# Kernel tuning notes

Hardware: AMD Instinct MI355X
Metric: run time of the kernel (lower is better)

Reference implementation:

```python
import jax, jax.numpy as jnp
import numpy as np

N_NODES = 100000
BN_EPS = 1e-5


def _gcn_layer(x, W, b, row, col, ew):
    # support = x @ W  (dense GEMM), then sparse aggregation: out[r] += w * support[c]
    support = x @ W
    msgs = ew[:, None] * support[col]            # [E, out_dim] gather
    agg = jax.ops.segment_sum(msgs, row, num_segments=N_NODES)
    return agg + b


def _batch_norm(x):
    # fresh BatchNorm1d each call: training-mode batch stats, gamma=1, beta=0
    mean = jnp.mean(x, axis=0, keepdims=True)
    var = jnp.var(x, axis=0, keepdims=True)      # biased variance, as in BN
    return (x - mean) * jax.lax.rsqrt(var + BN_EPS)


def setup_inputs() -> dict:
    key = jax.random.key(0)
    ks = jax.random.split(key, 10)
    nfeat, nhid, nclass = 512, 256, 64
    E = 3200000
    x = jax.random.normal(ks[0], (N_NODES, nfeat), dtype=jnp.float32)
    edge_index = jax.random.randint(ks[1], (2, E), 0, N_NODES, dtype=jnp.int32)
    edge_weight = jax.random.uniform(ks[2], (E,), dtype=jnp.float32)
    def glorot(k, fan_in, fan_out):
        s = 1.0 / np.sqrt(fan_in)
        return jax.random.uniform(k, (fan_in, fan_out), dtype=jnp.float32, minval=-s, maxval=s)
    W1 = glorot(ks[3], nfeat, nhid)
    b1 = jnp.zeros((nhid,), dtype=jnp.float32)
    W2 = glorot(ks[4], nhid, nhid)
    b2 = jnp.zeros((nhid,), dtype=jnp.float32)
    W3 = glorot(ks[5], nhid, nclass)
    b3 = jnp.zeros((nclass,), dtype=jnp.float32)
    return {"x": x, "edge_index": edge_index, "edge_weight": edge_weight,
            "W1": W1, "b1": b1, "W2": W2, "b2": b2, "W3": W3, "b3": b3}


def reference(x, edge_index, edge_weight, W1, b1, W2, b2, W3, b3):
    row, col = edge_index[0], edge_index[1]
    h = _batch_norm(jax.nn.relu(_gcn_layer(x, W1, b1, row, col, edge_weight)))
    h = _batch_norm(jax.nn.relu(_gcn_layer(h, W2, b2, row, col, edge_weight)))
    h = jax.nn.relu(_gcn_layer(h, W3, b3, row, col, edge_weight))
    return h
```

## Files before the change

kernel.cpp:

```cpp
#include <hip/hip_runtime.h>

#define THREADS 256
#define BSH 7
#define EPB 8192

typedef _Float16 f16;
typedef _Float16 f16x8 __attribute__((ext_vector_type(8)));
typedef _Float16 f16x4 __attribute__((ext_vector_type(4)));
typedef float f32x4 __attribute__((ext_vector_type(4)));


__global__ __launch_bounds__(256) void k_hist_convW(
    const int* __restrict__ rows, int* __restrict__ cnt2d, int e, int nblk, int nb,
    const float* __restrict__ W, f16* __restrict__ Wt, int K, int N,
    float* __restrict__ statZero, unsigned long long* __restrict__ tpub, int ntiles) {
  int t = threadIdx.x;
  if (blockIdx.x < nblk) {
    __shared__ int hist[1024];
    int blk = blockIdx.x;
    for (int i = t; i < nb; i += 256) hist[i] = 0;
    __syncthreads();
    int eb = blk * EPB;
#pragma unroll 4
    for (int it = 0; it < 32; ++it) {
      int i = eb + it * 256 + t;
      if (i < e) atomicAdd(&hist[rows[i] >> BSH], 1);
    }
    __syncthreads();
    for (int i = t; i < nb; i += 256) cnt2d[i * nblk + blk] = hist[i];
  } else {
    int cb = blockIdx.x - nblk;
    if (cb == 0) {
#pragma unroll
      for (int j = 0; j < 6; ++j) statZero[j * 256 + t] = 0.f;
      for (int i = t; i < ntiles; i += 256) tpub[i] = 0ULL;
    }
    int i = cb * 256 + t;
    if (i < N * K) {
      int n = i / K, k = i - n * K;
      Wt[i] = (f16)W[(size_t)k * N + n];
    }
  }
}


__global__ __launch_bounds__(256) void k_scanDL(
    const int* __restrict__ cnt, int* __restrict__ outp,
    unsigned long long* __restrict__ tpub, int n) {
  __shared__ int sh[256];
  __shared__ int sPrefix;
  int tile = blockIdx.x, t = threadIdx.x;
  int base = tile * 1024 + t * 4;
  int v[4];
#pragma unroll
  for (int j = 0; j < 4; ++j) {
    int idx = base + j;
    v[j] = (idx < n) ? cnt[idx] : 0;
  }
  int tot = v[0] + v[1] + v[2] + v[3];
  sh[t] = tot;
  __syncthreads();
  for (int off = 1; off < 256; off <<= 1) {
    int x = 0;
    if (t >= off) x = sh[t - off];
    __syncthreads();
    sh[t] += x;
    __syncthreads();
  }
  int blockTot = sh[255];
  int run = sh[t] - tot;

  if (t == 0) {
    if (tile == 0) {
      sPrefix = 0;
      atomicExch(&tpub[0], ((unsigned long long)(unsigned)blockTot << 2) | 2ULL);
    } else {
      atomicExch(&tpub[tile], ((unsigned long long)(unsigned)blockTot << 2) | 1ULL);
      long long sum = 0;
      int pred = tile - 1;
      while (true) {
        unsigned long long s = atomicAdd(&tpub[pred], 0ULL);
        unsigned st = (unsigned)(s & 3ULL);
        if (st == 2) { sum += (long long)(s >> 2); break; }
        if (st == 1) { sum += (long long)(s >> 2); --pred; }
      }
      sPrefix = (int)sum;
      atomicExch(&tpub[tile],
                 ((unsigned long long)(unsigned)(sum + blockTot) << 2) | 2ULL);
    }
  }
  __syncthreads();
  int pfx = sPrefix;
#pragma unroll
  for (int j = 0; j < 4; ++j) {
    int idx = base + j;
    if (idx < n) outp[idx] = run + pfx;
    run += v[j];
  }
  if (tile == gridDim.x - 1 && t == 0) outp[n] = pfx + blockTot;
}


template <int BN, bool AF16>
__device__ __forceinline__ void gemm_dev(
    int mblk, const void* __restrict__ Ap, const f16* __restrict__ Wt,
    const float* __restrict__ biasRow, f16* __restrict__ Csup, int M, int K,
    char* smem) {
  constexpr int BM = 128;
  constexpr int BK = 32;
  constexpr int LDT = BK + 8;
  f16 (*As)[LDT] = (f16(*)[LDT])smem;
  f16 (*Bs)[LDT] = (f16(*)[LDT])(smem + BM * LDT * 2);

  const int tid = threadIdx.x;
  const int wave = tid >> 6;
  const int lane = tid & 63;
  const int m0 = mblk * BM;
  constexpr int WM = (BN == 256) ? 8 : 2;
  constexpr int WN = 4;
  const int wrow = (BN == 256) ? 0 : wave * 32;
  const int wcol = (BN == 256) ? wave * 64 : 0;
  const int l15 = lane & 15;
  const int lq = lane >> 4;

  const int arow = tid >> 1;
  const int akofs = (tid & 1) * 16;
  const int srow = tid >> 2;
  const int skofs = (tid & 3) * 8;
  constexpr int BROWS = BN / 64;

  f32x4 acc[WM][WN] = {};

  for (int k0 = 0; k0 < K; k0 += BK) {
    f16x8 a16[2];
    int gr = m0 + arow;
    if constexpr (AF16) {
      if (gr < M) {
        const f16* ap = (const f16*)Ap + (size_t)gr * K + k0 + akofs;
        a16[0] = *(const f16x8*)ap;
        a16[1] = *(const f16x8*)(ap + 8);
      } else {
#pragma unroll
        for (int j = 0; j < 8; ++j) { a16[0][j] = (f16)0.f; a16[1][j] = (f16)0.f; }
      }
    } else {
      float va[16];
      if (gr < M) {
        const float* ap = (const float*)Ap + (size_t)gr * K + k0 + akofs;
#pragma unroll
        for (int q = 0; q < 4; ++q) *(float4*)&va[q * 4] = *(const float4*)(ap + q * 4);
      } else {
#pragma unroll
        for (int j = 0; j < 16; ++j) va[j] = 0.f;
      }
#pragma unroll
      for (int j = 0; j < 8; ++j) { a16[0][j] = (f16)va[j]; a16[1][j] = (f16)va[8 + j]; }
    }

    f16x8 vb[BROWS];
#pragma unroll
    for (int j = 0; j < BROWS; ++j)
      vb[j] = *(const f16x8*)(Wt + (size_t)(srow + j * 64) * K + k0 + skofs);

    __syncthreads();
    *(f16x8*)&As[arow][akofs] = a16[0];
    *(f16x8*)&As[arow][akofs + 8] = a16[1];
#pragma unroll
    for (int j = 0; j < BROWS; ++j) *(f16x8*)&Bs[srow + j * 64][skofs] = vb[j];
    __syncthreads();

    f16x8 af[WM], bf[WN];
#pragma unroll
    for (int m = 0; m < WM; ++m)
      af[m] = *(const f16x8*)&As[wrow + m * 16 + l15][lq * 8];
#pragma unroll
    for (int n = 0; n < WN; ++n)
      bf[n] = *(const f16x8*)&Bs[wcol + n * 16 + l15][lq * 8];
#pragma unroll
    for (int m = 0; m < WM; ++m)
#pragma unroll
      for (int n = 0; n < WN; ++n)
        acc[m][n] = __builtin_amdgcn_mfma_f32_16x16x32_f16(af[m], bf[n], acc[m][n], 0, 0, 0);
  }

  float bb[WN];
#pragma unroll
  for (int n = 0; n < WN; ++n)
    bb[n] = biasRow ? biasRow[wcol + n * 16 + l15] : 0.f;

#pragma unroll
  for (int m = 0; m < WM; ++m) {
#pragma unroll
    for (int r = 0; r < 4; ++r) {
      int row = m0 + wrow + m * 16 + lq * 4 + r;
      if (row < M) {
        f16* cp = Csup + (size_t)row * BN + wcol + l15;
#pragma unroll
        for (int n = 0; n < WN; ++n) cp[n * 16] = (f16)(acc[m][n][r] + bb[n]);
      }
    }
  }
}

template <int BN, bool AF16>
__global__ __launch_bounds__(256) void k_gemm_mfma(
    const void* __restrict__ Ap, const f16* __restrict__ Wt,
    const float* __restrict__ biasRow, f16* __restrict__ Csup, int M, int K) {
  __shared__ __align__(16) char smem[(128 + BN) * 40 * 2];
  gemm_dev<BN, AF16>(blockIdx.x, Ap, Wt, biasRow, Csup, M, K, smem);
}


__global__ __launch_bounds__(256) void k_bin_gemm(
    const int* __restrict__ rows, const int* __restrict__ cols,
    const float* __restrict__ w, const int* __restrict__ off2d,
    int2* __restrict__ temp, int e, int nblk, int nb,
    const float* __restrict__ x, const f16* __restrict__ Wt1,
    f16* __restrict__ sup, int M) {
  __shared__ __align__(16) char smem[(128 + 256) * 40 * 2];
  int t = threadIdx.x;
  if (blockIdx.x < nblk) {
    int* base = (int*)smem;
    int* cursor = (int*)smem + 1024;
    int blk = blockIdx.x;
    for (int i = t; i < nb; i += 256) {
      base[i] = off2d[i * nblk + blk];
      cursor[i] = 0;
    }
    __syncthreads();
    int eb = blk * EPB;
#pragma unroll 4
    for (int it = 0; it < 32; ++it) {
      int i = eb + it * 256 + t;
      if (i < e) {
        int r = rows[i];
        int b = r >> BSH;
        int pos = base[b] + atomicAdd(&cursor[b], 1);
        temp[pos] = make_int2(((r & 127) << 17) | cols[i], __float_as_int(w[i]));
      }
    }
  } else {
    gemm_dev<256, false>(blockIdx.x - nblk, x, Wt1, nullptr, sup, M, 512, smem);
  }
}


__global__ __launch_bounds__(256) void k_scatter(
    const int2* __restrict__ temp, const int* __restrict__ off2d,
    int* __restrict__ rowptr, int2* __restrict__ ed,
    int n, int e, int nblk, int nb) {
  __shared__ int rowCnt[128];
  __shared__ int rowBase[128];
  __shared__ int rowCur[128];
  int b = blockIdx.x, t = threadIdx.x;
  int r0 = b << BSH;
  int nr = min(128, n - r0);
  int start = off2d[b * nblk];
  int end = off2d[(b + 1) * nblk];
  if (t < 128) rowCnt[t] = 0;
  __syncthreads();
  for (int p = start + t; p < end; p += 256)
    atomicAdd(&rowCnt[temp[p].x >> 17], 1);
  __syncthreads();
  int v = 0;
  if (t < 128) {
    v = rowCnt[t];
    rowBase[t] = v;
  }
  __syncthreads();
  for (int off = 1; off < 128; off <<= 1) {
    int x = 0;
    if (t < 128 && t >= off) x = rowBase[t - off];
    __syncthreads();
    if (t < 128) rowBase[t] += x;
    __syncthreads();
  }
  if (t < 128) {
    int excl = rowBase[t] - v;
    rowBase[t] = excl;
    rowCur[t] = 0;
    if (t < nr) rowptr[r0 + t] = start + excl;
  }
  if (b == nb - 1 && t == 0) rowptr[n] = e;
  __syncthreads();
  for (int p = start + t; p < end; p += 256) {
    int2 ei = temp[p];
    int ro = ei.x >> 17;
    int slot = start + rowBase[ro] + atomicAdd(&rowCur[ro], 1);
    ed[slot] = make_int2(ei.x & 0x1FFFF, ei.y);
  }
}


__global__ __launch_bounds__(256) void k_bnfold(
    const float* __restrict__ W, const float* __restrict__ sums,
    f16* __restrict__ Wt, float* __restrict__ biasRow, int K, int N, int n) {
  __shared__ float sc[256], sf[256];
  int t = threadIdx.x;
  if (t < K) {
    float inv = 1.0f / (float)n;
    float mean = sums[t] * inv;
    float var = sums[256 + t] * inv - mean * mean;
    float rstd = rsqrtf(var + 1e-5f);
    sc[t] = rstd;
    sf[t] = -mean * rstd;
  }
  __syncthreads();
  int i = blockIdx.x * 256 + t;
  if (i < N * K) {
    int nn = i / K, k = i - nn * K;
    Wt[i] = (f16)(sc[k] * W[(size_t)k * N + nn]);
  }
  if (blockIdx.x < (K >> 4) && t < N) {
    int k0 = blockIdx.x * 16;
    float s = 0.f;
#pragma unroll
    for (int j = 0; j < 16; ++j) s += sf[k0 + j] * W[(size_t)(k0 + j) * N + t];
    atomicAdd(&biasRow[t], s);
  }
}


__global__ __launch_bounds__(256) void k_agg256(
    const f16* __restrict__ sup, const int* __restrict__ rowptr,
    const int2* __restrict__ ed, const float* __restrict__ bias,
    f16* __restrict__ out, int n) {
  int wid = (blockIdx.x * THREADS + threadIdx.x) >> 6;
  int lane = threadIdx.x & 63;
  if (wid >= n) return;
  int p0 = rowptr[wid], p1 = rowptr[wid + 1];

  const f16x4* supv = (const f16x4*)sup;
  float acc[4][4] = {};
  int p = p0;
  for (; p + 16 <= p1; p += 16) {
    int2 e[16];
#pragma unroll
    for (int j = 0; j < 16; ++j) e[j] = ed[p + j];
    f16x4 v[16];
#pragma unroll
    for (int j = 0; j < 16; ++j) v[j] = supv[(size_t)e[j].x * 64 + lane];
#pragma unroll
    for (int j = 0; j < 16; ++j) {
      float wt = __int_as_float(e[j].y);
      acc[j & 3][0] += wt * (float)v[j][0];
      acc[j & 3][1] += wt * (float)v[j][1];
      acc[j & 3][2] += wt * (float)v[j][2];
      acc[j & 3][3] += wt * (float)v[j][3];
    }
  }
  for (; p + 4 <= p1; p += 4) {
    int2 e[4];
#pragma unroll
    for (int j = 0; j < 4; ++j) e[j] = ed[p + j];
    f16x4 v[4];
#pragma unroll
    for (int j = 0; j < 4; ++j) v[j] = supv[(size_t)e[j].x * 64 + lane];
#pragma unroll
    for (int j = 0; j < 4; ++j) {
      float wt = __int_as_float(e[j].y);
      acc[j][0] += wt * (float)v[j][0];
      acc[j][1] += wt * (float)v[j][1];
      acc[j][2] += wt * (float)v[j][2];
      acc[j][3] += wt * (float)v[j][3];
    }
  }
  for (; p < p1; ++p) {
    int2 e0 = ed[p];
    float wt = __int_as_float(e0.y);
    f16x4 v = supv[(size_t)e0.x * 64 + lane];
    acc[0][0] += wt * (float)v[0];
    acc[0][1] += wt * (float)v[1];
    acc[0][2] += wt * (float)v[2];
    acc[0][3] += wt * (float)v[3];
  }
  float4 b = *(const float4*)(bias + lane * 4);
  f16x4 r;
  r[0] = (f16)fmaxf(acc[0][0] + acc[1][0] + acc[2][0] + acc[3][0] + b.x, 0.f);
  r[1] = (f16)fmaxf(acc[0][1] + acc[1][1] + acc[2][1] + acc[3][1] + b.y, 0.f);
  r[2] = (f16)fmaxf(acc[0][2] + acc[1][2] + acc[2][2] + acc[3][2] + b.z, 0.f);
  r[3] = (f16)fmaxf(acc[0][3] + acc[1][3] + acc[2][3] + acc[3][3] + b.w, 0.f);
  *(f16x4*)(out + (size_t)wid * 256 + lane * 4) = r;
}


__global__ __launch_bounds__(256) void k_agg64(
    const f16* __restrict__ sup, const int* __restrict__ rowptr,
    const int2* __restrict__ ed, const float* __restrict__ bias,
    float* __restrict__ out, int n) {
  int wid = (blockIdx.x * THREADS + threadIdx.x) >> 6;
  int lane = threadIdx.x & 63;
  if (wid >= n) return;
  int p0 = rowptr[wid], p1 = rowptr[wid + 1];
  int q = lane >> 4;
  int hl = lane & 15;

  const f16x4* supv = (const f16x4*)sup;
  float acc[2][4] = {};
  int p = p0;
  for (; p + 32 <= p1; p += 32) {
    int2 e[8];
#pragma unroll
    for (int j = 0; j < 8; ++j) e[j] = ed[p + 4 * j + q];
    f16x4 v[8];
#pragma unroll
    for (int j = 0; j < 8; ++j) v[j] = supv[(size_t)e[j].x * 16 + hl];
#pragma unroll
    for (int j = 0; j < 8; ++j) {
      float wt = __int_as_float(e[j].y);
      acc[j & 1][0] += wt * (float)v[j][0];
      acc[j & 1][1] += wt * (float)v[j][1];
      acc[j & 1][2] += wt * (float)v[j][2];
      acc[j & 1][3] += wt * (float)v[j][3];
    }
  }
  for (; p + 4 <= p1; p += 4) {
    int2 e0 = ed[p + q];
    float wt = __int_as_float(e0.y);
    f16x4 v = supv[(size_t)e0.x * 16 + hl];
    acc[0][0] += wt * (float)v[0];
    acc[0][1] += wt * (float)v[1];
    acc[0][2] += wt * (float)v[2];
    acc[0][3] += wt * (float)v[3];
  }
  if (p < p1) {
    int idx = p + q;
    int c = 0;
    float wt = 0.f;
    if (idx < p1) {
      int2 e0 = ed[idx];
      c = e0.x;
      wt = __int_as_float(e0.y);
    }
    f16x4 v = supv[(size_t)c * 16 + hl];
    acc[0][0] += wt * (float)v[0];
    acc[0][1] += wt * (float)v[1];
    acc[0][2] += wt * (float)v[2];
    acc[0][3] += wt * (float)v[3];
  }
  float t0 = acc[0][0] + acc[1][0];
  float t1 = acc[0][1] + acc[1][1];
  float t2 = acc[0][2] + acc[1][2];
  float t3 = acc[0][3] + acc[1][3];
  t0 += __shfl_xor(t0, 16); t0 += __shfl_xor(t0, 32);
  t1 += __shfl_xor(t1, 16); t1 += __shfl_xor(t1, 32);
  t2 += __shfl_xor(t2, 16); t2 += __shfl_xor(t2, 32);
  t3 += __shfl_xor(t3, 16); t3 += __shfl_xor(t3, 32);
  if (q == 0) {
    float4 b = *(const float4*)(bias + hl * 4);
    float4 res;
    res.x = fmaxf(t0 + b.x, 0.f);
    res.y = fmaxf(t1 + b.y, 0.f);
    res.z = fmaxf(t2 + b.z, 0.f);
    res.w = fmaxf(t3 + b.w, 0.f);
    *(float4*)(out + (size_t)wid * 64 + hl * 4) = res;
  }
}


__global__ __launch_bounds__(256) void k_colstats(const f16* __restrict__ y,
                                                  float* __restrict__ sums, int n) {
  __shared__ float sh[8][256];
  int t = threadIdx.x;
  int cg = (t & 31) * 8;
  int rs = t >> 5;
  float s[8] = {}, s2[8] = {};
  for (int r = blockIdx.x * 8 + rs; r < n; r += gridDim.x * 8) {
    f16x8 v = *(const f16x8*)(y + (size_t)r * 256 + cg);
#pragma unroll
    for (int j = 0; j < 8; ++j) {
      float f = (float)v[j];
      s[j] += f;
      s2[j] += f * f;
    }
  }
#pragma unroll
  for (int j = 0; j < 8; ++j) sh[rs][cg + j] = s[j];
  __syncthreads();
  float tot = 0.f;
#pragma unroll
  for (int k = 0; k < 8; ++k) tot += sh[k][t];
  atomicAdd(&sums[t], tot);
  __syncthreads();
#pragma unroll
  for (int j = 0; j < 8; ++j) sh[rs][cg + j] = s2[j];
  __syncthreads();
  tot = 0.f;
#pragma unroll
  for (int k = 0; k < 8; ++k) tot += sh[k][t];
  atomicAdd(&sums[256 + t], tot);
}


extern "C" void kernel_launch(void* const* d_in, const int* in_sizes, int n_in,
                              void* d_out, int out_size, void* d_ws, size_t ws_size,
                              hipStream_t stream) {
  const float* x = (const float*)d_in[0];
  const int* ei = (const int*)d_in[1];
  const float* ew = (const float*)d_in[2];
  const float* W1 = (const float*)d_in[3];
  const float* b1 = (const float*)d_in[4];
  const float* W2 = (const float*)d_in[5];
  const float* b2 = (const float*)d_in[6];
  const float* W3 = (const float*)d_in[7];
  const float* b3 = (const float*)d_in[8];
  float* out = (float*)d_out;

  const int N = in_sizes[0] / 512;
  const int E = in_sizes[2];

  const int NB = (N + 127) >> BSH;
  const int NBLK = (E + EPB - 1) / EPB;
  const int scanN = NB * NBLK;
  const int ntiles = (scanN + 1023) / 1024;

  char* p = (char*)d_ws;
  auto alloc = [&](size_t bytes) {
    void* r = (void*)p;
    p += (bytes + 255) & ~(size_t)255;
    return r;
  };
  int* rowptr = (int*)alloc((size_t)(N + 1) * 4);
  int* cnt2d = (int*)alloc((size_t)scanN * 4);
  int* off2d = (int*)alloc((size_t)(scanN + 1) * 4);
  unsigned long long* tpub = (unsigned long long*)alloc((size_t)ntiles * 8);
  float* statZ = (float*)alloc(1536 * 4);
  float* sumsA = statZ;
  float* sumsB = statZ + 512;
  float* biasRowA = statZ + 1024;
  float* biasRowB = statZ + 1280;
  f16* Wt1 = (f16*)alloc((size_t)512 * 256 * 2);
  f16* Wt2 = (f16*)alloc((size_t)256 * 256 * 2);
  f16* Wt3 = (f16*)alloc((size_t)256 * 64 * 2);
  int2* temp = (int2*)alloc((size_t)E * 8);
  int2* ed = (int2*)alloc((size_t)E * 8);
  f16* sup = (f16*)alloc((size_t)N * 256 * 2);
  f16* act = (f16*)alloc((size_t)N * 256 * 2);

  const int* rows = ei;
  const int* colsIn = ei + E;

  const int gemmBlocks = (N + 127) / 128;
  const int aggBlocks = (N * 64 + THREADS - 1) / THREADS;
  const int convBlocks = (512 * 256 + 255) / 256;

  k_hist_convW<<<NBLK + convBlocks, 256, 0, stream>>>(
      rows, cnt2d, E, NBLK, NB, W1, Wt1, 512, 256, statZ, tpub, ntiles);

  k_scanDL<<<ntiles, 256, 0, stream>>>(cnt2d, off2d, tpub, scanN);

  k_bin_gemm<<<NBLK + gemmBlocks, 256, 0, stream>>>(
      rows, colsIn, ew, off2d, temp, E, NBLK, NB, x, Wt1, sup, N);

  k_scatter<<<NB, 256, 0, stream>>>(temp, off2d, rowptr, ed, N, E, NBLK, NB);

  k_agg256<<<aggBlocks, 256, 0, stream>>>(sup, rowptr, ed, b1, act, N);

  k_colstats<<<240, 256, 0, stream>>>(act, sumsA, N);
  k_bnfold<<<(256 * 256 + 255) / 256, 256, 0, stream>>>(W2, sumsA, Wt2, biasRowA, 256, 256, N);

  k_gemm_mfma<256, true><<<gemmBlocks, 256, 0, stream>>>(act, Wt2, biasRowA, sup, N, 256);
  k_agg256<<<aggBlocks, 256, 0, stream>>>(sup, rowptr, ed, b2, act, N);

  k_colstats<<<240, 256, 0, stream>>>(act, sumsB, N);
  k_bnfold<<<(256 * 64 + 255) / 256, 256, 0, stream>>>(W3, sumsB, Wt3, biasRowB, 256, 64, N);

  k_gemm_mfma<64, true><<<gemmBlocks, 256, 0, stream>>>(act, Wt3, biasRowB, sup, N, 256);
  k_agg64<<<aggBlocks, 256, 0, stream>>>(sup, rowptr, ed, b3, out, N);
}
```

Before: 873.4 us.

## Fuse BN column stats into aggregation and apply BN normalization in GEMM A-load

The aggregation kernel now reduces per-column sum and sum-of-squares within each block and adds them atomically, which removes the separate colstats pass over the activation. The bnfold kernel is also removed. The GEMM instead computes per-column scale and shift from those sums and applies them to the A tile as it loads, and all three weight conversions move into the front kernel. This cuts four launches and one full read of the activations, at the cost of about 2x512 atomics per aggregation block and extra per-element ALU work plus shared-memory reads in the GEMM load path.

```diff
diff --git a/kernel.cpp b/kernel.cpp
--- a/kernel.cpp
+++ b/kernel.cpp
@@ -10,9 +10,11 @@
 typedef float f32x4 __attribute__((ext_vector_type(4)));
 
 
-__global__ __launch_bounds__(256) void k_hist_convW(
+__global__ __launch_bounds__(256) void k_front(
     const int* __restrict__ rows, int* __restrict__ cnt2d, int e, int nblk, int nb,
-    const float* __restrict__ W, f16* __restrict__ Wt, int K, int N,
+    const float* __restrict__ W1, f16* __restrict__ Wt1,
+    const float* __restrict__ W2, f16* __restrict__ Wt2,
+    const float* __restrict__ W3, f16* __restrict__ Wt3,
     float* __restrict__ statZero, unsigned long long* __restrict__ tpub, int ntiles) {
   int t = threadIdx.x;
   if (blockIdx.x < nblk) {
@@ -32,13 +34,21 @@
     int cb = blockIdx.x - nblk;
     if (cb == 0) {
 #pragma unroll
-      for (int j = 0; j < 6; ++j) statZero[j * 256 + t] = 0.f;
+      for (int j = 0; j < 4; ++j) statZero[j * 256 + t] = 0.f;
       for (int i = t; i < ntiles; i += 256) tpub[i] = 0ULL;
     }
-    int i = cb * 256 + t;
-    if (i < N * K) {
-      int n = i / K, k = i - n * K;
-      Wt[i] = (f16)W[(size_t)k * N + n];
+    if (cb < 512) {
+      int i = cb * 256 + t;
+      int n = i >> 9, k = i & 511;
+      Wt1[i] = (f16)W1[(size_t)k * 256 + n];
+    } else if (cb < 768) {
+      int i = (cb - 512) * 256 + t;
+      int n = i >> 8, k = i & 255;
+      Wt2[i] = (f16)W2[(size_t)k * 256 + n];
+    } else {
+      int i = (cb - 768) * 256 + t;
+      int n = i >> 8, k = i & 255;
+      Wt3[i] = (f16)W3[(size_t)k * 64 + n];
     }
   }
 }
@@ -101,16 +111,17 @@
 }
 
 
-template <int BN, bool AF16>
+template <int BN, bool AF16, bool BNF>
 __device__ __forceinline__ void gemm_dev(
     int mblk, const void* __restrict__ Ap, const f16* __restrict__ Wt,
-    const float* __restrict__ biasRow, f16* __restrict__ Csup, int M, int K,
-    char* smem) {
+    f16* __restrict__ Csup, int M, int K,
+    const float* __restrict__ sums, int nrows, char* smem) {
   constexpr int BM = 128;
   constexpr int BK = 32;
   constexpr int LDT = BK + 8;
   f16 (*As)[LDT] = (f16(*)[LDT])smem;
   f16 (*Bs)[LDT] = (f16(*)[LDT])(smem + BM * LDT * 2);
+  __shared__ float scL[256], sfL[256];
 
   const int tid = threadIdx.x;
   const int wave = tid >> 6;
@@ -129,6 +140,16 @@
   const int skofs = (tid & 3) * 8;
   constexpr int BROWS = BN / 64;
 
+  if constexpr (BNF) {
+    float inv = 1.0f / (float)nrows;
+    float mean = sums[tid] * inv;
+    float var = sums[256 + tid] * inv - mean * mean;
+    float rstd = rsqrtf(var + 1e-5f);
+    scL[tid] = rstd;
+    sfL[tid] = -mean * rstd;
+    __syncthreads();
+  }
+
   f32x4 acc[WM][WN] = {};
 
   for (int k0 = 0; k0 < K; k0 += BK) {
@@ -139,6 +160,15 @@
         const f16* ap = (const f16*)Ap + (size_t)gr * K + k0 + akofs;
         a16[0] = *(const f16x8*)ap;
         a16[1] = *(const f16x8*)(ap + 8);
+        if constexpr (BNF) {
+#pragma unroll
+          for (int h = 0; h < 2; ++h)
+#pragma unroll
+            for (int j = 0; j < 8; ++j) {
+              int k = k0 + akofs + h * 8 + j;
+              a16[h][j] = (f16)((float)a16[h][j] * scL[k] + sfL[k]);
+            }
+        }
       } else {
 #pragma unroll
         for (int j = 0; j < 8; ++j) { a16[0][j] = (f16)0.f; a16[1][j] = (f16)0.f; }
@@ -183,11 +213,6 @@
         acc[m][n] = __builtin_amdgcn_mfma_f32_16x16x32_f16(af[m], bf[n], acc[m][n], 0, 0, 0);
   }
 
-  float bb[WN];
-#pragma unroll
-  for (int n = 0; n < WN; ++n)
-    bb[n] = biasRow ? biasRow[wcol + n * 16 + l15] : 0.f;
-
 #pragma unroll
   for (int m = 0; m < WM; ++m) {
 #pragma unroll
@@ -196,18 +221,19 @@
       if (row < M) {
         f16* cp = Csup + (size_t)row * BN + wcol + l15;
 #pragma unroll
-        for (int n = 0; n < WN; ++n) cp[n * 16] = (f16)(acc[m][n][r] + bb[n]);
+        for (int n = 0; n < WN; ++n) cp[n * 16] = (f16)acc[m][n][r];
       }
     }
   }
 }
 
-template <int BN, bool AF16>
+template <int BN, bool AF16, bool BNF>
 __global__ __launch_bounds__(256) void k_gemm_mfma(
     const void* __restrict__ Ap, const f16* __restrict__ Wt,
-    const float* __restrict__ biasRow, f16* __restrict__ Csup, int M, int K) {
+    f16* __restrict__ Csup, int M, int K,
+    const float* __restrict__ sums, int nrows) {
   __shared__ __align__(16) char smem[(128 + BN) * 40 * 2];
-  gemm_dev<BN, AF16>(blockIdx.x, Ap, Wt, biasRow, Csup, M, K, smem);
+  gemm_dev<BN, AF16, BNF>(blockIdx.x, Ap, Wt, Csup, M, K, sums, nrows, smem);
 }
 
 
@@ -240,7 +266,7 @@
       }
     }
   } else {
-    gemm_dev<256, false>(blockIdx.x - nblk, x, Wt1, nullptr, sup, M, 512, smem);
+    gemm_dev<256, false, false>(blockIdx.x - nblk, x, Wt1, sup, M, 512, nullptr, 0, smem);
   }
 }
 
@@ -292,43 +318,18 @@
 }
 
 
-__global__ __launch_bounds__(256) void k_bnfold(
-    const float* __restrict__ W, const float* __restrict__ sums,
-    f16* __restrict__ Wt, float* __restrict__ biasRow, int K, int N, int n) {
-  __shared__ float sc[256], sf[256];
-  int t = threadIdx.x;
-  if (t < K) {
-    float inv = 1.0f / (float)n;
-    float mean = sums[t] * inv;
-    float var = sums[256 + t] * inv - mean * mean;
-    float rstd = rsqrtf(var + 1e-5f);
-    sc[t] = rstd;
-    sf[t] = -mean * rstd;
-  }
-  __syncthreads();
-  int i = blockIdx.x * 256 + t;
-  if (i < N * K) {
-    int nn = i / K, k = i - nn * K;
-    Wt[i] = (f16)(sc[k] * W[(size_t)k * N + nn]);
-  }
-  if (blockIdx.x < (K >> 4) && t < N) {
-    int k0 = blockIdx.x * 16;
-    float s = 0.f;
-#pragma unroll
-    for (int j = 0; j < 16; ++j) s += sf[k0 + j] * W[(size_t)(k0 + j) * N + t];
-    atomicAdd(&biasRow[t], s);
-  }
-}
-
-
 __global__ __launch_bounds__(256) void k_agg256(
     const f16* __restrict__ sup, const int* __restrict__ rowptr,
     const int2* __restrict__ ed, const float* __restrict__ bias,
-    f16* __restrict__ out, int n) {
-  int wid = (blockIdx.x * THREADS + threadIdx.x) >> 6;
-  int lane = threadIdx.x & 63;
-  if (wid >= n) return;
-  int p0 = rowptr[wid], p1 = rowptr[wid + 1];
+    f16* __restrict__ out, float* __restrict__ sums, int n) {
+  __shared__ float shs[4][256];
+  int tid = threadIdx.x;
+  int wave = tid >> 6;
+  int wid = (blockIdx.x * THREADS + tid) >> 6;
+  int lane = tid & 63;
+  bool valid = wid < n;
+  int p0 = 0, p1 = 0;
+  if (valid) { p0 = rowptr[wid]; p1 = rowptr[wid + 1]; }
 
   const f16x4* supv = (const f16x4*)sup;
   float acc[4][4] = {};
@@ -375,12 +376,26 @@
     acc[0][3] += wt * (float)v[3];
   }
   float4 b = *(const float4*)(bias + lane * 4);
-  f16x4 r;
-  r[0] = (f16)fmaxf(acc[0][0] + acc[1][0] + acc[2][0] + acc[3][0] + b.x, 0.f);
-  r[1] = (f16)fmaxf(acc[0][1] + acc[1][1] + acc[2][1] + acc[3][1] + b.y, 0.f);
-  r[2] = (f16)fmaxf(acc[0][2] + acc[1][2] + acc[2][2] + acc[3][2] + b.z, 0.f);
-  r[3] = (f16)fmaxf(acc[0][3] + acc[1][3] + acc[2][3] + acc[3][3] + b.w, 0.f);
-  *(f16x4*)(out + (size_t)wid * 256 + lane * 4) = r;
+  float r0 = 0.f, r1 = 0.f, r2 = 0.f, r3 = 0.f;
+  if (valid) {
+    r0 = fmaxf(acc[0][0] + acc[1][0] + acc[2][0] + acc[3][0] + b.x, 0.f);
+    r1 = fmaxf(acc[0][1] + acc[1][1] + acc[2][1] + acc[3][1] + b.y, 0.f);
+    r2 = fmaxf(acc[0][2] + acc[1][2] + acc[2][2] + acc[3][2] + b.z, 0.f);
+    r3 = fmaxf(acc[0][3] + acc[1][3] + acc[2][3] + acc[3][3] + b.w, 0.f);
+    f16x4 r;
+    r[0] = (f16)r0; r[1] = (f16)r1; r[2] = (f16)r2; r[3] = (f16)r3;
+    *(f16x4*)(out + (size_t)wid * 256 + lane * 4) = r;
+  }
+  *(float4*)&shs[wave][lane * 4] = make_float4(r0, r1, r2, r3);
+  __syncthreads();
+  float s = shs[0][tid] + shs[1][tid] + shs[2][tid] + shs[3][tid];
+  __syncthreads();
+  *(float4*)&shs[wave][lane * 4] =
+      make_float4(r0 * r0, r1 * r1, r2 * r2, r3 * r3);
+  __syncthreads();
+  float s2 = shs[0][tid] + shs[1][tid] + shs[2][tid] + shs[3][tid];
+  atomicAdd(&sums[tid], s);
+  atomicAdd(&sums[256 + tid], s2);
 }
 
 
@@ -458,40 +473,6 @@
 }
 
 
-__global__ __launch_bounds__(256) void k_colstats(const f16* __restrict__ y,
-                                                  float* __restrict__ sums, int n) {
-  __shared__ float sh[8][256];
-  int t = threadIdx.x;
-  int cg = (t & 31) * 8;
-  int rs = t >> 5;
-  float s[8] = {}, s2[8] = {};
-  for (int r = blockIdx.x * 8 + rs; r < n; r += gridDim.x * 8) {
-    f16x8 v = *(const f16x8*)(y + (size_t)r * 256 + cg);
-#pragma unroll
-    for (int j = 0; j < 8; ++j) {
-      float f = (float)v[j];
-      s[j] += f;
-      s2[j] += f * f;
-    }
-  }
-#pragma unroll
-  for (int j = 0; j < 8; ++j) sh[rs][cg + j] = s[j];
-  __syncthreads();
-  float tot = 0.f;
-#pragma unroll
-  for (int k = 0; k < 8; ++k) tot += sh[k][t];
-  atomicAdd(&sums[t], tot);
-  __syncthreads();
-#pragma unroll
-  for (int j = 0; j < 8; ++j) sh[rs][cg + j] = s2[j];
-  __syncthreads();
-  tot = 0.f;
-#pragma unroll
-  for (int k = 0; k < 8; ++k) tot += sh[k][t];
-  atomicAdd(&sums[256 + t], tot);
-}
-
-
 extern "C" void kernel_launch(void* const* d_in, const int* in_sizes, int n_in,
                               void* d_out, int out_size, void* d_ws, size_t ws_size,
                               hipStream_t stream) {
@@ -524,11 +505,9 @@
   int* cnt2d = (int*)alloc((size_t)scanN * 4);
   int* off2d = (int*)alloc((size_t)(scanN + 1) * 4);
   unsigned long long* tpub = (unsigned long long*)alloc((size_t)ntiles * 8);
-  float* statZ = (float*)alloc(1536 * 4);
+  float* statZ = (float*)alloc(1024 * 4);
   float* sumsA = statZ;
   float* sumsB = statZ + 512;
-  float* biasRowA = statZ + 1024;
-  float* biasRowB = statZ + 1280;
   f16* Wt1 = (f16*)alloc((size_t)512 * 256 * 2);
   f16* Wt2 = (f16*)alloc((size_t)256 * 256 * 2);
   f16* Wt3 = (f16*)alloc((size_t)256 * 64 * 2);
@@ -542,10 +521,9 @@
 
   const int gemmBlocks = (N + 127) / 128;
   const int aggBlocks = (N * 64 + THREADS - 1) / THREADS;
-  const int convBlocks = (512 * 256 + 255) / 256;
-
-  k_hist_convW<<<NBLK + convBlocks, 256, 0, stream>>>(
-      rows, cnt2d, E, NBLK, NB, W1, Wt1, 512, 256, statZ, tpub, ntiles);
+
+  k_front<<<NBLK + 832, 256, 0, stream>>>(
+      rows, cnt2d, E, NBLK, NB, W1, Wt1, W2, Wt2, W3, Wt3, statZ, tpub, ntiles);
 
   k_scanDL<<<ntiles, 256, 0, stream>>>(cnt2d, off2d, tpub, scanN);
 
@@ -554,17 +532,13 @@
 
   k_scatter<<<NB, 256, 0, stream>>>(temp, off2d, rowptr, ed, N, E, NBLK, NB);
 
-  k_agg256<<<aggBlocks, 256, 0, stream>>>(sup, rowptr, ed, b1, act, N);
-
-  k_colstats<<<240, 256, 0, stream>>>(act, sumsA, N);
-  k_bnfold<<<(256 * 256 + 255) / 256, 256, 0, stream>>>(W2, sumsA, Wt2, biasRowA, 256, 256, N);
-
-  k_gemm_mfma<256, true><<<gemmBlocks, 256, 0, stream>>>(act, Wt2, biasRowA, sup, N, 256);
-  k_agg256<<<aggBlocks, 256, 0, stream>>>(sup, rowptr, ed, b2, act, N);
-
-  k_colstats<<<240, 256, 0, stream>>>(act, sumsB, N);
-  k_bnfold<<<(256 * 64 + 255) / 256, 256, 0, stream>>>(W3, sumsB, Wt3, biasRowB, 256, 64, N);
-
-  k_gemm_mfma<64, true><<<gemmBlocks, 256, 0, stream>>>(act, Wt3, biasRowB, sup, N, 256);
+  k_agg256<<<aggBlocks, 256, 0, stream>>>(sup, rowptr, ed, b1, act, sumsA, N);
+
+  k_gemm_mfma<256, true, true><<<gemmBlocks, 256, 0, stream>>>(
+      act, Wt2, sup, N, 256, sumsA, N);
+  k_agg256<<<aggBlocks, 256, 0, stream>>>(sup, rowptr, ed, b2, act, sumsB, N);
+
+  k_gemm_mfma<64, true, true><<<gemmBlocks, 256, 0, stream>>>(
+      act, Wt3, sup, N, 256, sumsB, N);
   k_agg64<<<aggBlocks, 256, 0, stream>>>(sup, rowptr, ed, b3, out, N);
 }
```

New measurement: 1.639 ms. +87.7%, slower.
